# Optimization experiments

Hardware: AMD Instinct MI355X
Metric: run time of the kernel (lower is better)

Reference implementation:

```python
import jax, jax.numpy as jnp
import numpy as np

N_NODES = 65536
N_GRAPHS = 64


def gcn_conv(x, W, b, src, dst, n):
    # PyG GCNConv: add self-loops, symmetric normalization D^-1/2 (A+I) D^-1/2, then linear.
    xw = x @ W  # [N, F_out]
    deg = jnp.zeros((n,), x.dtype).at[dst].add(1.0) + 1.0  # +1 for self-loop
    dinv = jax.lax.rsqrt(deg)
    norm = dinv[src] * dinv[dst]  # [E]
    agg = jnp.zeros_like(xw).at[dst].add(xw[src] * norm[:, None])
    agg = agg + xw * (dinv * dinv)[:, None]  # self-loop term, norm_ii = 1/deg_i
    return agg + b


def setup_inputs() -> dict:
    key = jax.random.key(0)
    ks = jax.random.split(key, 8)
    E = 524288
    x = jax.random.normal(ks[0], (N_NODES, 1), jnp.float32)
    edge_index = jax.random.randint(ks[1], (2, E), 0, N_NODES, dtype=jnp.int64)
    batch = jnp.sort(jax.random.randint(ks[2], (N_NODES,), 0, N_GRAPHS, dtype=jnp.int64))
    def glorot(k, fi, fo):
        s = np.sqrt(2.0 / (fi + fo)).astype(np.float32)
        return jax.random.normal(k, (fi, fo), jnp.float32) * s
    return {
        "x": x, "edge_index": edge_index, "batch": batch,
        "W1": glorot(ks[3], 1, 128), "b1": jnp.zeros((128,), jnp.float32),
        "W2": glorot(ks[4], 128, 64), "b2": jnp.zeros((64,), jnp.float32),
        "W3": glorot(ks[5], 64, 32), "b3": jnp.zeros((32,), jnp.float32),
        "Wfc": glorot(ks[6], 32, 10), "bfc": jnp.zeros((10,), jnp.float32),
    }


def reference(x, edge_index, batch, W1, b1, W2, b2, W3, b3, Wfc, bfc):
    src, dst = edge_index[0], edge_index[1]
    n = x.shape[0]
    h = jax.nn.relu(gcn_conv(x, W1, b1, src, dst, n))
    # dropout is identity in eval mode
    h = jax.nn.relu(gcn_conv(h, W2, b2, src, dst, n))
    h = jax.nn.relu(gcn_conv(h, W3, b3, src, dst, n))
    # global mean pool per graph
    sums = jax.ops.segment_sum(h, batch, num_segments=N_GRAPHS)  # [B, 32]
    cnts = jax.ops.segment_sum(jnp.ones((n,), h.dtype), batch, num_segments=N_GRAPHS)
    pooled = sums / jnp.maximum(cnts, 1.0)[:, None]
    return pooled @ Wfc + bfc  # [B, 10]
```

## Files before the change

### kernel.cpp

```cpp
#include <hip/hip_runtime.h>
#include <hip/hip_fp16.h>

#define THREADS 256

typedef union { uint2 u; __half2 h[2]; } H4;
typedef union { uint4 u; __half2 h[4]; } H8;


__global__ void k_count(const int* __restrict__ dst, int* __restrict__ counts,
                        int* __restrict__ seq, int E) {
    int t = blockIdx.x * blockDim.x + threadIdx.x;
    if (t < E) seq[t] = atomicAdd(&counts[dst[t]], 1);
}

__global__ void k_scan1(const int* __restrict__ counts, const float* __restrict__ x,
                        float* __restrict__ dinv, float* __restrict__ s1,
                        int* __restrict__ rowloc, int* __restrict__ blocksums) {
    __shared__ int s[256];
    int i = blockIdx.x * 256 + threadIdx.x;
    int c = counts[i];
    float d = rsqrtf((float)c + 1.0f);
    dinv[i] = d;
    s1[i] = x[i] * d;
    s[threadIdx.x] = c;
    __syncthreads();
    for (int off = 1; off < 256; off <<= 1) {
        int v = (threadIdx.x >= off) ? s[threadIdx.x - off] : 0;
        __syncthreads();
        s[threadIdx.x] += v;
        __syncthreads();
    }
    rowloc[i] = s[threadIdx.x] - c;
    if (threadIdx.x == 255) blocksums[blockIdx.x] = s[255];
}

__global__ void k_fill(const int* __restrict__ src, const int* __restrict__ dst,
                       const int* __restrict__ rowloc, const int* __restrict__ seq,
                       const int* __restrict__ blocksums,
                       int* __restrict__ esrc, int* __restrict__ rowstart, int E) {
    __shared__ int boff[256];
    {
        int c = blocksums[threadIdx.x];
        boff[threadIdx.x] = c;
        __syncthreads();
        for (int off = 1; off < 256; off <<= 1) {
            int v = (threadIdx.x >= off) ? boff[threadIdx.x - off] : 0;
            __syncthreads();
            boff[threadIdx.x] += v;
            __syncthreads();
        }
        boff[threadIdx.x] -= c;
        __syncthreads();
    }
    int e = blockIdx.x * blockDim.x + threadIdx.x;
    if (e < E) {
        int d = dst[e];
        esrc[rowloc[d] + boff[d >> 8] + seq[e]] = src[e];
    }
    if (blockIdx.x < 256) {
        int i = blockIdx.x * 256 + threadIdx.x;
        rowstart[i] = rowloc[i] + boff[blockIdx.x];
    }
}

#define L12_R 8
__global__ void k_l1l2(const float* __restrict__ s1, const float* __restrict__ dinv,
                       const int* __restrict__ rowstart, const int* __restrict__ counts,
                       const int* __restrict__ esrc,
                       const float* __restrict__ W1, const float* __restrict__ b1,
                       const float* __restrict__ W2, __half* __restrict__ xws2, int N) {
    __shared__ float wb[128 * 2];
    __shared__ float W2s[128 * 64];
    __shared__ float als[128];
    __shared__ float dls[128];
    for (int idx = threadIdx.x; idx < 128; idx += 256) {
        wb[idx * 2] = W1[idx];
        wb[idx * 2 + 1] = b1[idx];
    }
    for (int idx = threadIdx.x; idx < 128 * 64 / 4; idx += 256)
        reinterpret_cast<float4*>(W2s)[idx] = reinterpret_cast<const float4*>(W2)[idx];
    if (threadIdx.x < 128) {
        int i = blockIdx.x * 128 + threadIdx.x;
        float a = 0.f, di = 0.f;
        if (i < N) {
            di = dinv[i];
            float t = s1[i];
            int p = rowstart[i], end = p + counts[i];
            for (; p + 3 < end; p += 4) {
                int a0 = esrc[p], a1 = esrc[p + 1], a2 = esrc[p + 2], a3 = esrc[p + 3];
                float v0 = s1[a0], v1 = s1[a1], v2 = s1[a2], v3 = s1[a3];
                t += (v0 + v1) + (v2 + v3);
            }
            for (; p < end; ++p) t += s1[esrc[p]];
            a = di * t;
        }
        als[threadIdx.x] = a;
        dls[threadIdx.x] = di;
    }
    __syncthreads();

    int c4 = threadIdx.x & 15;
    int rg = threadIdx.x >> 4;
    int base = blockIdx.x * 128 + rg * L12_R;

    float a[L12_R];
#pragma unroll
    for (int r = 0; r < L12_R; ++r) a[r] = als[rg * L12_R + r];

    float4 acc[L12_R] = {};
    for (int k = 0; k < 128; ++k) {
        float2 w1b1 = *reinterpret_cast<const float2*>(&wb[k * 2]);
        float4 w2 = *reinterpret_cast<const float4*>(&W2s[k * 64 + c4 * 4]);
#pragma unroll
        for (int r = 0; r < L12_R; ++r) {
            float h = fmaxf(fmaf(a[r], w1b1.x, w1b1.y), 0.f);
            acc[r].x = fmaf(h, w2.x, acc[r].x);
            acc[r].y = fmaf(h, w2.y, acc[r].y);
            acc[r].z = fmaf(h, w2.z, acc[r].z);
            acc[r].w = fmaf(h, w2.w, acc[r].w);
        }
    }
#pragma unroll
    for (int r = 0; r < L12_R; ++r) {
        int i = base + r;
        if (i < N) {
            float di = dls[rg * L12_R + r];
            H4 o;
            o.h[0] = __floats2half2_rn(acc[r].x * di, acc[r].y * di);
            o.h[1] = __floats2half2_rn(acc[r].z * di, acc[r].w * di);
            reinterpret_cast<uint2*>(xws2)[(size_t)i * 16 + c4] = o.u;
        }
    }
}

__global__ void k_l2l3(const int* __restrict__ rowstart, const int* __restrict__ counts,
                       const int* __restrict__ esrc, const __half* __restrict__ xws2,
                       const float* __restrict__ dinv, const float* __restrict__ b2,
                       const float* __restrict__ W3, __half* __restrict__ xws3, int N) {
    __shared__ float W3s[64 * 32];
    __shared__ float h2s[32][68];
    __shared__ float b2s[64];
    for (int idx = threadIdx.x; idx < 64 * 32 / 4; idx += 256)
        reinterpret_cast<float4*>(W3s)[idx] = reinterpret_cast<const float4*>(W3)[idx];
    if (threadIdx.x < 64) b2s[threadIdx.x] = b2[threadIdx.x];
    __syncthreads();

    {
        int c8 = threadIdx.x & 7;
        int r  = threadIdx.x >> 3;
        int i  = blockIdx.x * 32 + r;
        if (i < N) {
            const uint4* x4 = reinterpret_cast<const uint4*>(xws2);
            H8 p; p.u = x4[(size_t)i * 8 + c8];
            float acc[8];
#pragma unroll
            for (int j = 0; j < 4; ++j) {
                float2 f = __half22float2(p.h[j]);
                acc[2 * j] = f.x; acc[2 * j + 1] = f.y;
            }
            int q = rowstart[i], end = q + counts[i];
            for (; q + 3 < end; q += 4) {
                int sa = esrc[q], sb = esrc[q + 1], sc = esrc[q + 2], sd = esrc[q + 3];
                H8 pa, pb, pc, pd;
                pa.u = x4[(size_t)sa * 8 + c8];
                pb.u = x4[(size_t)sb * 8 + c8];
                pc.u = x4[(size_t)sc * 8 + c8];
                pd.u = x4[(size_t)sd * 8 + c8];
#pragma unroll
                for (int j = 0; j < 4; ++j) {
                    float2 fa = __half22float2(pa.h[j]);
                    float2 fb = __half22float2(pb.h[j]);
                    float2 fc = __half22float2(pc.h[j]);
                    float2 fd = __half22float2(pd.h[j]);
                    acc[2 * j]     += (fa.x + fb.x) + (fc.x + fd.x);
                    acc[2 * j + 1] += (fa.y + fb.y) + (fc.y + fd.y);
                }
            }
            for (; q < end; ++q) {
                H8 pe; pe.u = x4[(size_t)esrc[q] * 8 + c8];
#pragma unroll
                for (int j = 0; j < 4; ++j) {
                    float2 f = __half22float2(pe.h[j]);
                    acc[2 * j] += f.x; acc[2 * j + 1] += f.y;
                }
            }
            float di = dinv[i];
            float4 hv0, hv1;
            float* hv = &hv0.x;
#pragma unroll
            for (int j = 0; j < 8; ++j)
                (j < 4 ? (&hv0.x)[j] : (&hv1.x)[j - 4]) =
                    fmaxf(fmaf(di, acc[j], b2s[c8 * 8 + j]), 0.f);
            (void)hv;
            *reinterpret_cast<float4*>(&h2s[r][c8 * 8])     = hv0;
            *reinterpret_cast<float4*>(&h2s[r][c8 * 8 + 4]) = hv1;
        }
    }
    __syncthreads();
    {
        int c  = threadIdx.x & 7;
        int r2 = threadIdx.x >> 3;
        int i2 = blockIdx.x * 32 + r2;
        if (i2 >= N) return;
        float4 acc = {};
#pragma unroll
        for (int k = 0; k < 64; ++k) {
            float h = h2s[r2][k];
            float4 w = *reinterpret_cast<const float4*>(&W3s[k * 32 + c * 4]);
            acc.x = fmaf(h, w.x, acc.x);
            acc.y = fmaf(h, w.y, acc.y);
            acc.z = fmaf(h, w.z, acc.z);
            acc.w = fmaf(h, w.w, acc.w);
        }
        float di = dinv[i2];
        H4 o;
        o.h[0] = __floats2half2_rn(acc.x * di, acc.y * di);
        o.h[1] = __floats2half2_rn(acc.z * di, acc.w * di);
        reinterpret_cast<uint2*>(xws3)[(size_t)i2 * 8 + c] = o.u;
    }
}

__global__ void k_l3pool(const int* __restrict__ rowstart, const int* __restrict__ counts,
                         const int* __restrict__ esrc, const __half* __restrict__ xws3,
                         const float* __restrict__ dinv, const float* __restrict__ b3,
                         const int* __restrict__ batch, float* __restrict__ sums,
                         float* __restrict__ cnt, int N) {
    __shared__ float sl[64 * 32];
    __shared__ float cl[64];
    for (int idx = threadIdx.x; idx < 64 * 32; idx += 256) sl[idx] = 0.f;
    if (threadIdx.x < 64) cl[threadIdx.x] = 0.f;
    __syncthreads();

    int c = threadIdx.x & 3;
    int r = threadIdx.x >> 2;
    int i = blockIdx.x * 64 + r;
    if (i < N) {
        const uint4* x4 = reinterpret_cast<const uint4*>(xws3);
        H8 p; p.u = x4[(size_t)i * 4 + c];
        float acc[8];
#pragma unroll
        for (int j = 0; j < 4; ++j) {
            float2 f = __half22float2(p.h[j]);
            acc[2 * j] = f.x; acc[2 * j + 1] = f.y;
        }
        int q = rowstart[i], end = q + counts[i];
        for (; q + 3 < end; q += 4) {
            int sa = esrc[q], sb = esrc[q + 1], sc = esrc[q + 2], sd = esrc[q + 3];
            H8 pa, pb, pc, pd;
            pa.u = x4[(size_t)sa * 4 + c];
            pb.u = x4[(size_t)sb * 4 + c];
            pc.u = x4[(size_t)sc * 4 + c];
            pd.u = x4[(size_t)sd * 4 + c];
#pragma unroll
            for (int j = 0; j < 4; ++j) {
                float2 fa = __half22float2(pa.h[j]);
                float2 fb = __half22float2(pb.h[j]);
                float2 fc = __half22float2(pc.h[j]);
                float2 fd = __half22float2(pd.h[j]);
                acc[2 * j]     += (fa.x + fb.x) + (fc.x + fd.x);
                acc[2 * j + 1] += (fa.y + fb.y) + (fc.y + fd.y);
            }
        }
        for (; q < end; ++q) {
            H8 pe; pe.u = x4[(size_t)esrc[q] * 4 + c];
#pragma unroll
            for (int j = 0; j < 4; ++j) {
                float2 f = __half22float2(pe.h[j]);
                acc[2 * j] += f.x; acc[2 * j + 1] += f.y;
            }
        }
        float di = dinv[i];
        int g = batch[i];
#pragma unroll
        for (int j = 0; j < 8; ++j)
            atomicAdd(&sl[g * 32 + c * 8 + j], fmaxf(fmaf(di, acc[j], b3[c * 8 + j]), 0.f));
        if (c == 0) atomicAdd(&cl[g], 1.f);
    }
    __syncthreads();

    int start = blockIdx.x * 64;
    if (start >= N) return;
    int g0 = batch[start];
    int g1 = batch[min(start + 63, N - 1)];
    int ng = g1 - g0 + 1;
    for (int idx = threadIdx.x; idx < ng * 32; idx += 256) {
        float v = sl[(g0 + idx / 32) * 32 + (idx & 31)];
        if (v != 0.f) atomicAdd(&sums[(g0 + idx / 32) * 32 + (idx & 31)], v);
    }
    for (int idx = threadIdx.x; idx < ng; idx += 256) {
        float v = cl[g0 + idx];
        if (v != 0.f) atomicAdd(&cnt[g0 + idx], v);
    }
}

__global__ void k_fc(const float* __restrict__ sums, const float* __restrict__ cnt,
                     const float* __restrict__ Wfc, const float* __restrict__ bfc,
                     float* __restrict__ out) {
    int t = blockIdx.x * blockDim.x + threadIdx.x;
    if (t >= 64 * 10) return;
    int g = t / 10, o = t % 10;
    float inv = 1.0f / fmaxf(cnt[g], 1.0f);
    float acc = bfc[o];
#pragma unroll
    for (int f = 0; f < 32; ++f) acc = fmaf(sums[g * 32 + f] * inv, Wfc[f * 10 + o], acc);
    out[t] = acc;
}

extern "C" void kernel_launch(void* const* d_in, const int* in_sizes, int n_in,
                              void* d_out, int out_size, void* d_ws, size_t ws_size,
                              hipStream_t stream) {
    const float* x    = (const float*)d_in[0];
    const int*   ei   = (const int*)d_in[1];
    const int*   batch= (const int*)d_in[2];
    const float* W1   = (const float*)d_in[3];
    const float* b1   = (const float*)d_in[4];
    const float* W2   = (const float*)d_in[5];
    const float* b2   = (const float*)d_in[6];
    const float* W3   = (const float*)d_in[7];
    const float* b3   = (const float*)d_in[8];
    const float* Wfc  = (const float*)d_in[9];
    const float* bfc  = (const float*)d_in[10];
    float* out = (float*)d_out;

    const int N = in_sizes[0];
    const int E = in_sizes[1] / 2;
    const int* src  = ei;
    const int* dstp = ei + E;

    char* ws = (char*)d_ws;
    size_t off = 0;
    auto alloc = [&](size_t bytes) { void* p = ws + off; off = (off + bytes + 15) & ~(size_t)15; return p; };
    int*    counts   = (int*)   alloc((size_t)N * 4);
    float*  sums     = (float*) alloc(64 * 32 * 4);
    float*  cnt      = (float*) alloc(64 * 4);
    size_t  zbytes   = (size_t)((char*)(cnt + 64) - (char*)counts);
    int*    rowloc   = (int*)   alloc((size_t)N * 4);
    int*    rowstart = (int*)   alloc((size_t)N * 4);
    int*    seq      = (int*)   alloc((size_t)E * 4);
    int*    blocksums= (int*)   alloc(256 * 4);
    int*    esrc     = (int*)   alloc((size_t)E * 4);
    float*  dinv     = (float*) alloc((size_t)N * 4);
    float*  s1       = (float*) alloc((size_t)N * 4);
    __half* xws2     = (__half*)alloc((size_t)N * 64 * 2);
    __half* xws3     = (__half*)alloc((size_t)N * 32 * 2);

    auto blocks = [](long n) { return (int)((n + THREADS - 1) / THREADS); };

    hipMemsetAsync(counts, 0, zbytes, stream);

    k_count<<<blocks(E), THREADS, 0, stream>>>(dstp, counts, seq, E);
    k_scan1<<<N / 256, 256, 0, stream>>>(counts, x, dinv, s1, rowloc, blocksums);
    k_fill <<<blocks(E), THREADS, 0, stream>>>(src, dstp, rowloc, seq, blocksums,
                                               esrc, rowstart, E);
    k_l1l2<<<(N + 127) / 128, THREADS, 0, stream>>>(s1, dinv, rowstart, counts, esrc,
                                                    W1, b1, W2, xws2, N);
    k_l2l3<<<(N + 31) / 32, THREADS, 0, stream>>>(rowstart, counts, esrc, xws2, dinv, b2, W3, xws3, N);
    k_l3pool<<<(N + 63) / 64, THREADS, 0, stream>>>(rowstart, counts, esrc, xws3, dinv, b3, batch,
                                                    sums, cnt, N);
    k_fc<<<blocks(640), THREADS, 0, stream>>>(sums, cnt, Wfc, bfc, out);
}
```

Before: 177.5 us.

## Replace layer-1 ReLU times W2 matmul with piecewise-linear lookup tables

Layer 1 has one input feature, so relu(a*W1+b1)@W2 is a piecewise-linear function of the scalar a. The new init kernel sorts the 128 ReLU breakpoints and precomputes slope/intercept tables for every interval. The layer-1/2 kernel then does a 7-step binary search and one FMA per output instead of a 128x64 inner product per node. The memset is folded into the init kernel and the gather loop is unrolled to 8, which adds a serial single-block setup kernel and can change float rounding order.

Result: slower. 217.2 us (+22.4%).

```diff
diff --git a/kernel.cpp b/kernel.cpp
--- a/kernel.cpp
+++ b/kernel.cpp
@@ -5,6 +5,59 @@
 
 typedef union { uint2 u; __half2 h[2]; } H4;
 typedef union { uint4 u; __half2 h[4]; } H8;
+
+__global__ void k_init(const float* __restrict__ W1, const float* __restrict__ b1,
+                       const float* __restrict__ W2,
+                       float* __restrict__ tsg, float* __restrict__ SA, float* __restrict__ SB,
+                       int* __restrict__ counts, float* __restrict__ sums, int N) {
+    if (blockIdx.x > 0) {
+        int i = (blockIdx.x - 1) * 256 + threadIdx.x;
+        if (i < N) counts[i] = 0;
+        return;
+    }
+    __shared__ float tval[128];
+    __shared__ float ts[128];
+    __shared__ int widx[128];
+    for (int idx = threadIdx.x; idx < 64 * 32 + 64; idx += 256) sums[idx] = 0.f;
+    if (threadIdx.x < 128) {
+        float w = W1[threadIdx.x];
+        tval[threadIdx.x] = (w != 0.f) ? (-b1[threadIdx.x] / w) : __builtin_inff();
+    }
+    __syncthreads();
+    if (threadIdx.x < 128) {
+        float t = tval[threadIdx.x];
+        int r = 0;
+        for (int j = 0; j < 128; ++j) {
+            float tj = tval[j];
+            r += (tj < t || (tj == t && j < (int)threadIdx.x)) ? 1 : 0;
+        }
+        ts[r] = t;
+        widx[r] = threadIdx.x;
+    }
+    __syncthreads();
+    if (threadIdx.x < 128) tsg[threadIdx.x] = ts[threadIdx.x];
+    if (threadIdx.x < 64) {
+        int c = threadIdx.x;
+        float negA = 0.f, negB = 0.f, constB = 0.f;
+        for (int r = 0; r < 128; ++r) {
+            int k = widx[r];
+            float w = W1[k], b = b1[k], w2 = W2[k * 64 + c];
+            if (w < 0.f) { negA += w * w2; negB += b * w2; }
+            else if (w == 0.f && b > 0.f) constB += b * w2;
+        }
+        float posA = 0.f, posB = 0.f, nA = 0.f, nB = 0.f;
+        SA[c] = negA;
+        SB[c] = negB + constB;
+        for (int r = 0; r < 128; ++r) {
+            int k = widx[r];
+            float w = W1[k], b = b1[k], w2 = W2[k * 64 + c];
+            if (w > 0.f) { posA += w * w2; posB += b * w2; }
+            else if (w < 0.f) { nA += w * w2; nB += b * w2; }
+            SA[(r + 1) * 64 + c] = posA + (negA - nA);
+            SB[(r + 1) * 64 + c] = posB + (negB - nB) + constB;
+        }
+    }
+}
 
 
 __global__ void k_count(const int* __restrict__ dst, int* __restrict__ counts,
@@ -63,35 +116,35 @@
     }
 }
 
-#define L12_R 8
 __global__ void k_l1l2(const float* __restrict__ s1, const float* __restrict__ dinv,
                        const int* __restrict__ rowstart, const int* __restrict__ counts,
                        const int* __restrict__ esrc,
-                       const float* __restrict__ W1, const float* __restrict__ b1,
-                       const float* __restrict__ W2, __half* __restrict__ xws2, int N) {
-    __shared__ float wb[128 * 2];
-    __shared__ float W2s[128 * 64];
+                       const float* __restrict__ tsg, const float* __restrict__ SA,
+                       const float* __restrict__ SB, __half* __restrict__ xws2, int N) {
+    __shared__ float tsl[128];
     __shared__ float als[128];
     __shared__ float dls[128];
-    for (int idx = threadIdx.x; idx < 128; idx += 256) {
-        wb[idx * 2] = W1[idx];
-        wb[idx * 2 + 1] = b1[idx];
-    }
-    for (int idx = threadIdx.x; idx < 128 * 64 / 4; idx += 256)
-        reinterpret_cast<float4*>(W2s)[idx] = reinterpret_cast<const float4*>(W2)[idx];
+    if (threadIdx.x < 128) tsl[threadIdx.x] = tsg[threadIdx.x];
     if (threadIdx.x < 128) {
         int i = blockIdx.x * 128 + threadIdx.x;
         float a = 0.f, di = 0.f;
         if (i < N) {
             di = dinv[i];
             float t = s1[i];
-            int p = rowstart[i], end = p + counts[i];
-            for (; p + 3 < end; p += 4) {
-                int a0 = esrc[p], a1 = esrc[p + 1], a2 = esrc[p + 2], a3 = esrc[p + 3];
+            int q = rowstart[i], end = q + counts[i];
+            for (; q + 7 < end; q += 8) {
+                int a0 = esrc[q], a1 = esrc[q + 1], a2 = esrc[q + 2], a3 = esrc[q + 3];
+                int a4 = esrc[q + 4], a5 = esrc[q + 5], a6 = esrc[q + 6], a7 = esrc[q + 7];
+                float v0 = s1[a0], v1 = s1[a1], v2 = s1[a2], v3 = s1[a3];
+                float v4 = s1[a4], v5 = s1[a5], v6 = s1[a6], v7 = s1[a7];
+                t += ((v0 + v1) + (v2 + v3)) + ((v4 + v5) + (v6 + v7));
+            }
+            for (; q + 3 < end; q += 4) {
+                int a0 = esrc[q], a1 = esrc[q + 1], a2 = esrc[q + 2], a3 = esrc[q + 3];
                 float v0 = s1[a0], v1 = s1[a1], v2 = s1[a2], v3 = s1[a3];
                 t += (v0 + v1) + (v2 + v3);
             }
-            for (; p < end; ++p) t += s1[esrc[p]];
+            for (; q < end; ++q) t += s1[esrc[q]];
             a = di * t;
         }
         als[threadIdx.x] = a;
@@ -101,35 +154,25 @@
 
     int c4 = threadIdx.x & 15;
     int rg = threadIdx.x >> 4;
-    int base = blockIdx.x * 128 + rg * L12_R;
-
-    float a[L12_R];
-#pragma unroll
-    for (int r = 0; r < L12_R; ++r) a[r] = als[rg * L12_R + r];
-
-    float4 acc[L12_R] = {};
-    for (int k = 0; k < 128; ++k) {
-        float2 w1b1 = *reinterpret_cast<const float2*>(&wb[k * 2]);
-        float4 w2 = *reinterpret_cast<const float4*>(&W2s[k * 64 + c4 * 4]);
-#pragma unroll
-        for (int r = 0; r < L12_R; ++r) {
-            float h = fmaxf(fmaf(a[r], w1b1.x, w1b1.y), 0.f);
-            acc[r].x = fmaf(h, w2.x, acc[r].x);
-            acc[r].y = fmaf(h, w2.y, acc[r].y);
-            acc[r].z = fmaf(h, w2.z, acc[r].z);
-            acc[r].w = fmaf(h, w2.w, acc[r].w);
-        }
-    }
-#pragma unroll
-    for (int r = 0; r < L12_R; ++r) {
-        int i = base + r;
-        if (i < N) {
-            float di = dls[rg * L12_R + r];
-            H4 o;
-            o.h[0] = __floats2half2_rn(acc[r].x * di, acc[r].y * di);
-            o.h[1] = __floats2half2_rn(acc[r].z * di, acc[r].w * di);
-            reinterpret_cast<uint2*>(xws2)[(size_t)i * 16 + c4] = o.u;
-        }
+#pragma unroll
+    for (int rr = 0; rr < 8; ++rr) {
+        int lr = rg * 8 + rr;
+        int row = blockIdx.x * 128 + lr;
+        if (row >= N) break;
+        float av = als[lr];
+        int lo = 0, hi = 128;
+#pragma unroll
+        for (int it = 0; it < 7; ++it) {
+            int m = (lo + hi) >> 1;
+            if (tsl[m] <= av) lo = m + 1; else hi = m;
+        }
+        float4 sa = *reinterpret_cast<const float4*>(&SA[lo * 64 + c4 * 4]);
+        float4 sb = *reinterpret_cast<const float4*>(&SB[lo * 64 + c4 * 4]);
+        float dv = dls[lr];
+        H4 o;
+        o.h[0] = __floats2half2_rn(fmaf(av, sa.x, sb.x) * dv, fmaf(av, sa.y, sb.y) * dv);
+        o.h[1] = __floats2half2_rn(fmaf(av, sa.z, sb.z) * dv, fmaf(av, sa.w, sb.w) * dv);
+        reinterpret_cast<uint2*>(xws2)[(size_t)row * 16 + c4] = o.u;
     }
 }
 
@@ -185,13 +228,12 @@
                 }
             }
             float di = dinv[i];
-            float4 hv0, hv1;
-            float* hv = &hv0.x;
+            float hv[8];
 #pragma unroll
             for (int j = 0; j < 8; ++j)
-                (j < 4 ? (&hv0.x)[j] : (&hv1.x)[j - 4]) =
-                    fmaxf(fmaf(di, acc[j], b2s[c8 * 8 + j]), 0.f);
-            (void)hv;
+                hv[j] = fmaxf(fmaf(di, acc[j], b2s[c8 * 8 + j]), 0.f);
+            float4 hv0 = {hv[0], hv[1], hv[2], hv[3]};
+            float4 hv1 = {hv[4], hv[5], hv[6], hv[7]};
             *reinterpret_cast<float4*>(&h2s[r][c8 * 8])     = hv0;
             *reinterpret_cast<float4*>(&h2s[r][c8 * 8 + 4]) = hv1;
         }
@@ -331,9 +373,8 @@
     size_t off = 0;
     auto alloc = [&](size_t bytes) { void* p = ws + off; off = (off + bytes + 15) & ~(size_t)15; return p; };
     int*    counts   = (int*)   alloc((size_t)N * 4);
-    float*  sums     = (float*) alloc(64 * 32 * 4);
-    float*  cnt      = (float*) alloc(64 * 4);
-    size_t  zbytes   = (size_t)((char*)(cnt + 64) - (char*)counts);
+    float*  sums     = (float*) alloc(64 * 32 * 4 + 64 * 4);
+    float*  cnt      = sums + 64 * 32;
     int*    rowloc   = (int*)   alloc((size_t)N * 4);
     int*    rowstart = (int*)   alloc((size_t)N * 4);
     int*    seq      = (int*)   alloc((size_t)E * 4);
@@ -341,19 +382,21 @@
     int*    esrc     = (int*)   alloc((size_t)E * 4);
     float*  dinv     = (float*) alloc((size_t)N * 4);
     float*  s1       = (float*) alloc((size_t)N * 4);
+    float*  tsg      = (float*) alloc(128 * 4);
+    float*  SA       = (float*) alloc(129 * 64 * 4);
+    float*  SB       = (float*) alloc(129 * 64 * 4);
     __half* xws2     = (__half*)alloc((size_t)N * 64 * 2);
     __half* xws3     = (__half*)alloc((size_t)N * 32 * 2);
 
     auto blocks = [](long n) { return (int)((n + THREADS - 1) / THREADS); };
 
-    hipMemsetAsync(counts, 0, zbytes, stream);
-
+    k_init <<<(N + 255) / 256 + 1, THREADS, 0, stream>>>(W1, b1, W2, tsg, SA, SB, counts, sums, N);
     k_count<<<blocks(E), THREADS, 0, stream>>>(dstp, counts, seq, E);
     k_scan1<<<N / 256, 256, 0, stream>>>(counts, x, dinv, s1, rowloc, blocksums);
     k_fill <<<blocks(E), THREADS, 0, stream>>>(src, dstp, rowloc, seq, blocksums,
                                                esrc, rowstart, E);
     k_l1l2<<<(N + 127) / 128, THREADS, 0, stream>>>(s1, dinv, rowstart, counts, esrc,
-                                                    W1, b1, W2, xws2, N);
+                                                    tsg, SA, SB, xws2, N);
     k_l2l3<<<(N + 31) / 32, THREADS, 0, stream>>>(rowstart, counts, esrc, xws2, dinv, b2, W3, xws3, N);
     k_l3pool<<<(N + 63) / 64, THREADS, 0, stream>>>(rowstart, counts, esrc, xws3, dinv, b3, batch,
                                                     sums, cnt, N);
```
